# Performance work log

Hardware: AMD Instinct MI355X
Metric: run time of the kernel (lower is better)

The kernel has to match this reference:

```python
import jax, jax.numpy as jnp
import numpy as np

B, TX, TY = 32, 64, 64
E = H = 1024
VEN = VCN = 32000


def _lstm_scan(x_gates, Whh, bhh, h0, c0):
    # x_gates: [T, B, 4H] precomputed input contribution (x @ Wih.T + bih)
    def step(carry, xg_t):
        h, c = carry
        gates = xg_t + h @ Whh.T + bhh  # [B, 4H]
        i, f, g, o = jnp.split(gates, 4, axis=-1)  # torch gate order i,f,g,o
        c = jax.nn.sigmoid(f) * c + jax.nn.sigmoid(i) * jnp.tanh(g)
        h = jax.nn.sigmoid(o) * jnp.tanh(c)
        return (h, c), (h, c)
    (hT, cT), (hs, cs) = jax.lax.scan(step, (h0, c0), x_gates)
    return hs, cs, hT, cT  # hs/cs: [T, B, H]


def setup_inputs() -> dict:
    key = jax.random.key(0)
    ks = jax.random.split(key, 12)
    u = lambda k, shp, s: jax.random.uniform(k, shp, jnp.float32, -s, s)
    s = 1.0 / np.sqrt(H)
    return {
        "x": jax.random.randint(ks[0], (B, TX), 0, VEN, dtype=jnp.int32),
        "x_mask": jnp.ones((B, TX), dtype=jnp.int32),
        "y": jax.random.randint(ks[1], (B, TY), 0, VCN, dtype=jnp.int32),
        "h0": jnp.zeros((B, H), jnp.float32),
        "c0": jnp.zeros((B, H), jnp.float32),
        "emb_en": u(ks[2], (VEN, E), 0.1),
        "emb_cn": u(ks[3], (VCN, E), 0.1),
        "Wih_e": u(ks[4], (4 * H, E), s),
        "Whh_e": u(ks[5], (4 * H, H), s),
        "bih_e": jnp.zeros((4 * H,), jnp.float32),
        "bhh_e": jnp.zeros((4 * H,), jnp.float32),
        "Wih_d": u(ks[6], (4 * H, E), s),
        "Whh_d": u(ks[7], (4 * H, H), s),
        "bih_d": jnp.zeros((4 * H,), jnp.float32),
        "bhh_d": jnp.zeros((4 * H,), jnp.float32),
        "Wout": u(ks[8], (VCN, H), 0.1),
        "bout": jnp.zeros((VCN,), jnp.float32),
    }


def reference(x, x_mask, y, h0, c0, emb_en, emb_cn,
              Wih_e, Whh_e, bih_e, bhh_e,
              Wih_d, Whh_d, bih_d, bhh_d, Wout, bout):
    # --- encoder: per-timestep LSTMCell unrolled via lax.scan ---
    xe = emb_en[x]  # [B, Tx, E]
    xg = jnp.einsum('bte,ge->tbg', xe, Wih_e) + bih_e  # [Tx, B, 4H]
    hs, cs, _, _ = _lstm_scan(xg, Whh_e, bhh_e, h0, c0)  # [Tx, B, H]
    # pick hidden/cell at last valid timestep (mask.sum - 1)
    lengths = jnp.sum(x_mask, axis=1) - 1  # [B]
    bidx = jnp.arange(x.shape[0])
    h = hs[lengths, bidx]  # [B, H]
    c = cs[lengths, bidx]
    # --- decoder: single-layer LSTM ---
    ye = emb_cn[y]  # [B, Ty, E]
    yg = jnp.einsum('bte,ge->tbg', ye, Wih_d) + bih_d  # [Ty, B, 4H]
    dh, _, _, _ = _lstm_scan(yg, Whh_d, bhh_d, h, c)  # [Ty, B, H]
    hiddens = jnp.transpose(dh, (1, 0, 2))  # [B, Ty, H]
    logits = jnp.einsum('bth,vh->btv', hiddens, Wout) + bout  # [B, Ty, V]
    decoded = jax.nn.log_softmax(logits, axis=-1)
    return decoded, hiddens
```

## Files before the change

### kernel.cpp

```cpp
#include <hip/hip_runtime.h>

typedef __attribute__((ext_vector_type(8))) short bf16x8;
typedef __attribute__((ext_vector_type(4))) float fx4;
typedef __attribute__((ext_vector_type(4))) unsigned short u16x4;
typedef __attribute__((ext_vector_type(8))) unsigned short u16x8;
typedef __attribute__((ext_vector_type(4))) unsigned int u32x4;

#define DEV static __device__ __forceinline__

DEV unsigned short f2bf(float f) {
  union { float f; unsigned u; } v; v.f = f;
  unsigned u = v.u;
  u += 0x7fffu + ((u >> 16) & 1u);
  return (unsigned short)(u >> 16);
}
DEV unsigned pk(float a, float b) { return (unsigned)f2bf(a) | ((unsigned)f2bf(b) << 16); }
DEV float sigm(float x) { return 1.f / (1.f + __expf(-x)); }

DEV u32x4 load_coh16(const void* p) {
  u32x4 r;
  asm volatile("global_load_dwordx4 %0, %1, off sc0 sc1" : "=v"(r) : "v"(p));
  return r;
}

__global__ void k_gather(const float* __restrict__ emb, const int* __restrict__ tok,
                         unsigned short* __restrict__ dst) {
  int r = blockIdx.x;
  int t = r >> 5, b = r & 31;
  int token = tok[b * 64 + t];
  const fx4* srow = (const fx4*)(emb + (long)token * 1024);
  u16x4* drow = (u16x4*)(dst + (long)r * 1024);
  fx4 v = srow[threadIdx.x];
  u16x4 o = { f2bf(v[0]), f2bf(v[1]), f2bf(v[2]), f2bf(v[3]) };
  drow[threadIdx.x] = o;
}

__global__ void k_lengths(const int* __restrict__ mask, int* __restrict__ sel) {
  int b = threadIdx.x;
  if (b < 32) {
    int s = 0;
    for (int t = 0; t < 64; ++t) s += mask[b * 64 + t];
    sel[b] = (s + 63) & 63;
  }
}

__global__ void k_init_state(const float* __restrict__ h, const float* __restrict__ c,
                             unsigned short* __restrict__ hbuf0, float* __restrict__ cbuf,
                             int* __restrict__ bar) {
  int i = blockIdx.x * 256 + threadIdx.x;
  hbuf0[i] = f2bf(h[i]);
  cbuf[i] = c[i];
  if (i < 4096) bar[i] = 0;
}

#define SCAN_NBLK 128

template<int MODE>
__global__ __launch_bounds__(512) void k_scan(
    const float* __restrict__ Whh,
    const float* __restrict__ bhh,
    const float* __restrict__ xg,
    unsigned short* __restrict__ hbuf,
    float* __restrict__ cbuf,
    const int* __restrict__ sel,
    float* __restrict__ hsel, float* __restrict__ csel,
    float* __restrict__ hid_out,
    unsigned short* __restrict__ hid_bf,
    int* __restrict__ bar) {
  __shared__ __align__(16) unsigned short hlds[49152];
  __shared__ float gbuf[2][2][32][16];
  int tid = threadIdx.x;
  int bid = blockIdx.x;
  int j0 = bid * 8;
  int w = tid >> 6, lane = tid & 63;
  int mt = w & 1, nt = (w >> 1) & 1, kh = w >> 2;
  int fr = lane & 15, fg = lane >> 4;
  unsigned* hbU = (unsigned*)hbuf;

  bf16x8 breg[16];
  {
    int r = nt * 16 + fr;
    const float* wrow = Whh + ((long)((r >> 3) * 1024 + j0 + (r & 7)) << 10);
#pragma unroll
    for (int i = 0; i < 16; ++i) {
      int kc = (kh * 16 + i) * 4 + fg;
      fx4 lo = *(const fx4*)(wrow + kc * 8);
      fx4 hi = *(const fx4*)(wrow + kc * 8 + 4);
      bf16x8 o = { (short)f2bf(lo[0]), (short)f2bf(lo[1]), (short)f2bf(lo[2]), (short)f2bf(lo[3]),
                   (short)f2bf(hi[0]), (short)f2bf(hi[1]), (short)f2bf(hi[2]), (short)f2bf(hi[3]) };
      breg[i] = o;
    }
  }

  int b = (tid & 255) >> 3, jj = tid & 7, j = j0 + jj;
  float bh0 = 0.f, bh1 = 0.f, bh2 = 0.f, bh3 = 0.f, c_reg = 0.f;
  float x0 = 0.f, x1 = 0.f, x2 = 0.f, x3 = 0.f;
  int sel_b = -1;
  if (tid < 256) {
    bh0 = bhh[j]; bh1 = bhh[1024 + j]; bh2 = bhh[2048 + j]; bh3 = bhh[3072 + j];
    c_reg = cbuf[b * 1024 + j];
    if (MODE == 0) sel_b = sel[b];
    const float* xp = xg + (long)b * 4096 + j;
    x0 = xp[0]; x1 = xp[1024]; x2 = xp[2048]; x3 = xp[3072];
  }

  for (int t = 0; t < 64; ++t) {
    const char* hsrc = (const char*)hbuf + (t & 1) * 65536;
    u32x4 hv[8];
#pragma unroll
    for (int it = 0; it < 8; ++it) {
      int c = it * 512 + tid;
      hv[it] = load_coh16(hsrc + (long)c * 16);
    }
    asm volatile("s_waitcnt vmcnt(0)" ::: "memory");
    __builtin_amdgcn_sched_barrier(0);
#pragma unroll
    for (int it = 0; it < 8; ++it) {
      int c = it * 512 + tid;
      int row = c >> 7, kc = c & 127;
      *(u16x8*)&hlds[(row * 128 + (kc ^ (row & 31))) * 8] = *(u16x8*)&hv[it];
    }
    __syncthreads();

    int arow = mt * 16 + fr;
    fx4 acca = {0.f, 0.f, 0.f, 0.f}, accb = {0.f, 0.f, 0.f, 0.f};
#pragma unroll
    for (int i = 0; i < 16; i += 2) {
      int kcA = (kh * 16 + i) * 4 + fg;
      int kcB = (kh * 16 + i + 1) * 4 + fg;
      bf16x8 a0 = *(const bf16x8*)&hlds[(arow * 128 + (kcA ^ (arow & 31))) * 8];
      bf16x8 a1 = *(const bf16x8*)&hlds[(arow * 128 + (kcB ^ (arow & 31))) * 8];
      acca = __builtin_amdgcn_mfma_f32_16x16x32_bf16(a0, breg[i], acca, 0, 0, 0);
      accb = __builtin_amdgcn_mfma_f32_16x16x32_bf16(a1, breg[i + 1], accb, 0, 0, 0);
    }
#pragma unroll
    for (int q = 0; q < 4; ++q)
      gbuf[kh][nt][mt * 16 + fg * 4 + q][fr] = acca[q] + accb[q];
    __syncthreads();

    if (tid < 256) {
      float gi = gbuf[0][0][b][jj]     + gbuf[1][0][b][jj]     + bh0 + x0;
      float gf = gbuf[0][0][b][8 + jj] + gbuf[1][0][b][8 + jj] + bh1 + x1;
      float gg = gbuf[0][1][b][jj]     + gbuf[1][1][b][jj]     + bh2 + x2;
      float go = gbuf[0][1][b][8 + jj] + gbuf[1][1][b][8 + jj] + bh3 + x3;
      float c_new = sigm(gf) * c_reg + sigm(gi) * tanhf(gg);
      float h = sigm(go) * tanhf(c_new);
      c_reg = c_new;
      float hp = __shfl_xor(h, 1);
      if ((jj & 1) == 0) {
        unsigned val = pk(h, hp);
        __hip_atomic_store(&hbU[((t & 1) ^ 1) * 16384 + b * 512 + ((j0 + jj) >> 1)], val,
                           __ATOMIC_RELAXED, __HIP_MEMORY_SCOPE_AGENT);
      }
      if (MODE == 0) {
        if (t == sel_b) { hsel[b * 1024 + j] = h; csel[b * 1024 + j] = c_new; }
      } else {
        long o = ((long)b * 64 + t) * 1024 + j;
        hid_out[o] = h;
        if (hid_bf) hid_bf[o] = f2bf(h);
      }
    }

    if (t < 63) {
      float nx0 = 0.f, nx1 = 0.f, nx2 = 0.f, nx3 = 0.f;
      if (tid < 256) {
        const float* xp = xg + (long)(t + 1) * 131072 + (long)b * 4096 + j;
        nx0 = xp[0]; nx1 = xp[1024]; nx2 = xp[2048]; nx3 = xp[3072];
      }
      __syncthreads();
      if (w == 0) {
        if (lane == 0)
          __hip_atomic_store(&bar[bid * 32], t + 1, __ATOMIC_RELAXED, __HIP_MEMORY_SCOPE_AGENT);
        for (;;) {
          int v0 = __hip_atomic_load(&bar[lane * 32], __ATOMIC_RELAXED, __HIP_MEMORY_SCOPE_AGENT);
          int v1 = __hip_atomic_load(&bar[(64 + lane) * 32], __ATOMIC_RELAXED, __HIP_MEMORY_SCOPE_AGENT);
          if (__ballot(v0 >= t + 1 && v1 >= t + 1) == 0xFFFFFFFFFFFFFFFFULL) break;
          __builtin_amdgcn_s_sleep(2);
        }
      }
      __syncthreads();
      x0 = nx0; x1 = nx1; x2 = nx2; x3 = nx3;
    }
  }
}

template<typename TA, typename TB>
__global__ __launch_bounds__(256) void k_gemm(const TA* __restrict__ A,
                                              const TB* __restrict__ Bw,
                                              const float* __restrict__ bias,
                                              float* __restrict__ C,
                                              int ldc, int q8) {
  __shared__ __align__(16) unsigned short As[2][4096];
  __shared__ __align__(16) unsigned short Bs[2][4096];
  int lid = blockIdx.x;
  int swz = (lid & 7) * q8 + (lid >> 3);
  long m0 = (long)(swz & 15) * 128;
  long n0 = (long)(swz >> 4) * 128;
  int tid = threadIdx.x, lane = tid & 63, w = tid >> 6;
  int mw = (w & 1) * 64, nw = (w >> 1) * 64;
  int fr = lane & 15, fg = lane >> 4;
  fx4 acc[4][4] = {};

  int crow[2], kc[2], phys[2];
#pragma unroll
  for (int u = 0; u < 2; ++u) {
    int c = tid + u * 256;
    crow[u] = c >> 2; kc[u] = c & 3;
    phys[u] = crow[u] * 4 + (kc[u] ^ ((crow[u] >> 1) & 3));
  }
  u32x4 ra[2], rb[2];
  auto loadOne = [&](const auto* P, long row, int u) -> u32x4 {
    long off = row * 1024 + kc[u] * 8;
    if constexpr (sizeof(*P) == 2) {
      return *(const u32x4*)(P + off);
    } else {
      fx4 lo = *(const fx4*)(P + off);
      fx4 hi = *(const fx4*)(P + off + 4);
      u32x4 r = { pk(lo[0], lo[1]), pk(lo[2], lo[3]), pk(hi[0], hi[1]), pk(hi[2], hi[3]) };
      return r;
    }
  };
  auto loadRegs = [&](int kt) {
#pragma unroll
    for (int u = 0; u < 2; ++u) {
      ra[u] = loadOne(A + (long)kt * 32, m0 + crow[u], u);
      rb[u] = loadOne(Bw + (long)kt * 32, n0 + crow[u], u);
    }
  };
  auto storeRegs = [&](int buf) {
#pragma unroll
    for (int u = 0; u < 2; ++u) {
      *(u32x4*)&As[buf][phys[u] * 8] = ra[u];
      *(u32x4*)&Bs[buf][phys[u] * 8] = rb[u];
    }
  };
  loadRegs(0);
  storeRegs(0);
  __syncthreads();
  for (int kt = 0; kt < 32; ++kt) {
    int cur = kt & 1;
    if (kt < 31) loadRegs(kt + 1);
    bf16x8 af[4], bf_[4];
#pragma unroll
    for (int mi = 0; mi < 4; ++mi) {
      int row = mw + mi * 16 + fr;
      af[mi] = *(const bf16x8*)&As[cur][(row * 4 + (fg ^ ((row >> 1) & 3))) * 8];
    }
#pragma unroll
    for (int ni = 0; ni < 4; ++ni) {
      int row = nw + ni * 16 + fr;
      bf_[ni] = *(const bf16x8*)&Bs[cur][(row * 4 + (fg ^ ((row >> 1) & 3))) * 8];
    }
#pragma unroll
    for (int mi = 0; mi < 4; ++mi)
#pragma unroll
      for (int ni = 0; ni < 4; ++ni)
        acc[mi][ni] = __builtin_amdgcn_mfma_f32_16x16x32_bf16(af[mi], bf_[ni], acc[mi][ni], 0, 0, 0);
    if (kt < 31) storeRegs((kt + 1) & 1);
    __syncthreads();
  }
#pragma unroll
  for (int ni = 0; ni < 4; ++ni) {
    long n = n0 + nw + ni * 16 + fr;
    float bs = bias[n];
#pragma unroll
    for (int mi = 0; mi < 4; ++mi) {
      long rbase = m0 + mw + mi * 16 + fg * 4;
#pragma unroll
      for (int q = 0; q < 4; ++q)
        C[(rbase + q) * ldc + n] = acc[mi][ni][q] + bs;
    }
  }
}

__global__ __launch_bounds__(256) void k_logsoftmax(float* __restrict__ logits) {
  long base = (long)blockIdx.x * 32000;
  float* row = logits + base;
  int tid = threadIdx.x;
  __shared__ float red[4];
  float m = -3.4e38f;
  for (int i = tid; i < 8000; i += 256) {
    fx4 v = ((const fx4*)row)[i];
    m = fmaxf(m, fmaxf(fmaxf(v[0], v[1]), fmaxf(v[2], v[3])));
  }
  for (int o = 32; o; o >>= 1) m = fmaxf(m, __shfl_xor(m, o));
  if ((tid & 63) == 0) red[tid >> 6] = m;
  __syncthreads();
  m = fmaxf(fmaxf(red[0], red[1]), fmaxf(red[2], red[3]));
  float s = 0.f;
  for (int i = tid; i < 8000; i += 256) {
    fx4 v = ((const fx4*)row)[i];
    s += __expf(v[0] - m) + __expf(v[1] - m) + __expf(v[2] - m) + __expf(v[3] - m);
  }
  for (int o = 32; o; o >>= 1) s += __shfl_xor(s, o);
  __syncthreads();
  if ((tid & 63) == 0) red[tid >> 6] = s;
  __syncthreads();
  float lse = m + logf(red[0] + red[1] + red[2] + red[3]);
  for (int i = tid; i < 8000; i += 256) {
    fx4 v = ((const fx4*)row)[i];
    fx4 o = { v[0] - lse, v[1] - lse, v[2] - lse, v[3] - lse };
    ((fx4*)row)[i] = o;
  }
}

extern "C" void kernel_launch(void* const* d_in, const int* in_sizes, int n_in,
                              void* d_out, int out_size, void* d_ws, size_t ws_size,
                              hipStream_t stream) {
  const int*   x     = (const int*)d_in[0];
  const int*   xmask = (const int*)d_in[1];
  const int*   y     = (const int*)d_in[2];
  const float* h0    = (const float*)d_in[3];
  const float* c0    = (const float*)d_in[4];
  const float* embE  = (const float*)d_in[5];
  const float* embC  = (const float*)d_in[6];
  const float* WihE  = (const float*)d_in[7];
  const float* WhhE  = (const float*)d_in[8];
  const float* bihE  = (const float*)d_in[9];
  const float* bhhE  = (const float*)d_in[10];
  const float* WihD  = (const float*)d_in[11];
  const float* WhhD  = (const float*)d_in[12];
  const float* bihD  = (const float*)d_in[13];
  const float* bhhD  = (const float*)d_in[14];
  const float* Wout  = (const float*)d_in[15];
  const float* bout  = (const float*)d_in[16];

  float* out = (float*)d_out;
  float* decoded = out;
  float* hiddens = out + 65536000L;

  float* xg_e = decoded;
  float* xg_d = decoded + 8388608L;
  unsigned short* xe_bf = (unsigned short*)(decoded + 16777216L);
  unsigned short* ye_bf = xe_bf + 2097152L;
  char* sp = (char*)(ye_bf + 2097152L);
  unsigned short* hbuf = (unsigned short*)sp; sp += 2 * 32768 * 2;
  float* cbuf = (float*)sp; sp += 32768 * 4;
  float* hsel = (float*)sp; sp += 32768 * 4;
  float* csel = (float*)sp; sp += 32768 * 4;
  int* sel = (int*)sp; sp += 256;
  int* bar = (int*)sp; sp += 16384;

  unsigned short* hid_bf = (unsigned short*)d_ws;
  bool fast = ws_size >= 2048L * 1024 * 2;

  k_gather<<<2048, 256, 0, stream>>>(embE, x, xe_bf);
  k_gather<<<2048, 256, 0, stream>>>(embC, y, ye_bf);
  k_lengths<<<1, 32, 0, stream>>>(xmask, sel);

  k_gemm<unsigned short, float><<<512, 256, 0, stream>>>(xe_bf, WihE, bihE, xg_e, 4096, 64);
  k_gemm<unsigned short, float><<<512, 256, 0, stream>>>(ye_bf, WihD, bihD, xg_d, 4096, 64);

  k_init_state<<<128, 256, 0, stream>>>(h0, c0, hbuf, cbuf, bar);
  k_scan<0><<<SCAN_NBLK, 512, 0, stream>>>(WhhE, bhhE, xg_e, hbuf, cbuf, sel,
                                           hsel, csel, nullptr, nullptr, bar);
  k_init_state<<<128, 256, 0, stream>>>(hsel, csel, hbuf, cbuf, bar);
  k_scan<1><<<SCAN_NBLK, 512, 0, stream>>>(WhhD, bhhD, xg_d, hbuf, cbuf, nullptr,
                                           nullptr, nullptr, hiddens,
                                           fast ? hid_bf : nullptr, bar);

  if (fast) k_gemm<unsigned short, float><<<4000, 256, 0, stream>>>(hid_bf, Wout, bout, decoded, 32000, 500);
  else      k_gemm<float, float><<<4000, 256, 0, stream>>>(hiddens, Wout, bout, decoded, 32000, 500);
  k_logsoftmax<<<2048, 256, 0, stream>>>(decoded);
}
```

Measured before the change: 1.016 ms.

## Pre-convert weights to bf16, add LDS-direct bf16 GEMM, online logsoftmax, pack barrier flags

Adds a kernel that converts the fp32 Wih and Wout weights to bf16 in scratch space. A new GEMM streams bf16 A and B tiles straight into LDS with global_load_lds, so the conversion no longer happens inside the GEMM loop. Log-softmax now uses a single-pass online max/sum reduction, cutting one full read of each logits row. The scan barrier flags are packed contiguously instead of padded 128 bytes apart, and the spin sleep is shortened. The weight conversion adds extra passes over the weights on every call, and the fast Wout path depends on a large enough workspace.

```diff
diff --git a/kernel.cpp b/kernel.cpp
--- a/kernel.cpp
+++ b/kernel.cpp
@@ -21,6 +21,22 @@
   u32x4 r;
   asm volatile("global_load_dwordx4 %0, %1, off sc0 sc1" : "=v"(r) : "v"(p));
   return r;
+}
+
+typedef __attribute__((address_space(1))) const unsigned int guint;
+typedef __attribute__((address_space(3))) unsigned int luint;
+DEV void gload_lds16(const void* g, void* l) {
+  __builtin_amdgcn_global_load_lds((guint*)g, (luint*)l, 16, 0, 0);
+}
+
+__global__ void k_f2bf4(const float* __restrict__ s, unsigned short* __restrict__ d, long n4) {
+  long i = (long)blockIdx.x * blockDim.x + threadIdx.x;
+  long st = (long)gridDim.x * blockDim.x;
+  for (; i < n4; i += st) {
+    fx4 v = ((const fx4*)s)[i];
+    u16x4 o = { f2bf(v[0]), f2bf(v[1]), f2bf(v[2]), f2bf(v[3]) };
+    ((u16x4*)d)[i] = o;
+  }
 }
 
 __global__ void k_gather(const float* __restrict__ emb, const int* __restrict__ tok,
@@ -170,16 +186,74 @@
       __syncthreads();
       if (w == 0) {
         if (lane == 0)
-          __hip_atomic_store(&bar[bid * 32], t + 1, __ATOMIC_RELAXED, __HIP_MEMORY_SCOPE_AGENT);
+          __hip_atomic_store(&bar[bid], t + 1, __ATOMIC_RELAXED, __HIP_MEMORY_SCOPE_AGENT);
         for (;;) {
-          int v0 = __hip_atomic_load(&bar[lane * 32], __ATOMIC_RELAXED, __HIP_MEMORY_SCOPE_AGENT);
-          int v1 = __hip_atomic_load(&bar[(64 + lane) * 32], __ATOMIC_RELAXED, __HIP_MEMORY_SCOPE_AGENT);
+          int v0 = __hip_atomic_load(&bar[lane], __ATOMIC_RELAXED, __HIP_MEMORY_SCOPE_AGENT);
+          int v1 = __hip_atomic_load(&bar[64 + lane], __ATOMIC_RELAXED, __HIP_MEMORY_SCOPE_AGENT);
           if (__ballot(v0 >= t + 1 && v1 >= t + 1) == 0xFFFFFFFFFFFFFFFFULL) break;
-          __builtin_amdgcn_s_sleep(2);
+          __builtin_amdgcn_s_sleep(1);
         }
       }
       __syncthreads();
       x0 = nx0; x1 = nx1; x2 = nx2; x3 = nx3;
+    }
+  }
+}
+
+__global__ __launch_bounds__(256) void k_gemm_bb(const unsigned short* __restrict__ A,
+                                                 const unsigned short* __restrict__ Bw,
+                                                 const float* __restrict__ bias,
+                                                 float* __restrict__ C,
+                                                 int ldc, int q8) {
+  __shared__ __align__(16) unsigned short As[2][4096];
+  __shared__ __align__(16) unsigned short Bs[2][4096];
+  int lid = blockIdx.x;
+  int swz = (lid & 7) * q8 + (lid >> 3);
+  long m0 = (long)(swz & 15) * 128;
+  long n0 = (long)(swz >> 4) * 128;
+  int tid = threadIdx.x, lane = tid & 63, w = tid >> 6;
+  int mw = (w & 1) * 64, nw = (w >> 1) * 64;
+  int fr = lane & 15, fg = lane >> 4;
+  fx4 acc[4][4] = {};
+  int c0 = tid, c1 = tid + 256;
+  const unsigned short* gA0 = A + (m0 + (c0 >> 2)) * 1024 + (c0 & 3) * 8;
+  const unsigned short* gA1 = A + (m0 + (c1 >> 2)) * 1024 + (c1 & 3) * 8;
+  const unsigned short* gB0 = Bw + (n0 + (c0 >> 2)) * 1024 + (c0 & 3) * 8;
+  const unsigned short* gB1 = Bw + (n0 + (c1 >> 2)) * 1024 + (c1 & 3) * 8;
+  auto stage = [&](int buf, int kt) {
+    int k0 = kt * 32;
+    gload_lds16(gA0 + k0, &As[buf][c0 * 8]);
+    gload_lds16(gA1 + k0, &As[buf][c1 * 8]);
+    gload_lds16(gB0 + k0, &Bs[buf][c0 * 8]);
+    gload_lds16(gB1 + k0, &Bs[buf][c1 * 8]);
+  };
+  stage(0, 0);
+  __syncthreads();
+  for (int kt = 0; kt < 32; ++kt) {
+    int cur = kt & 1;
+    if (kt < 31) stage(cur ^ 1, kt + 1);
+    bf16x8 af[4], bfr[4];
+#pragma unroll
+    for (int mi = 0; mi < 4; ++mi) af[mi]  = *(const bf16x8*)&As[cur][(mw + mi * 16 + fr) * 32 + fg * 8];
+#pragma unroll
+    for (int ni = 0; ni < 4; ++ni) bfr[ni] = *(const bf16x8*)&Bs[cur][(nw + ni * 16 + fr) * 32 + fg * 8];
+#pragma unroll
+    for (int mi = 0; mi < 4; ++mi)
+#pragma unroll
+      for (int ni = 0; ni < 4; ++ni)
+        acc[mi][ni] = __builtin_amdgcn_mfma_f32_16x16x32_bf16(af[mi], bfr[ni], acc[mi][ni], 0, 0, 0);
+    __syncthreads();
+  }
+#pragma unroll
+  for (int ni = 0; ni < 4; ++ni) {
+    long n = n0 + nw + ni * 16 + fr;
+    float bs = bias[n];
+#pragma unroll
+    for (int mi = 0; mi < 4; ++mi) {
+      long rbase = m0 + mw + mi * 16 + fg * 4;
+#pragma unroll
+      for (int q = 0; q < 4; ++q)
+        C[(rbase + q) * ldc + n] = acc[mi][ni][q] + bs;
     }
   }
 }
@@ -277,26 +351,26 @@
   long base = (long)blockIdx.x * 32000;
   float* row = logits + base;
   int tid = threadIdx.x;
-  __shared__ float red[4];
-  float m = -3.4e38f;
+  __shared__ float redm[4], reds[4];
+  float m = -3.4e38f, s = 0.f;
   for (int i = tid; i < 8000; i += 256) {
     fx4 v = ((const fx4*)row)[i];
-    m = fmaxf(m, fmaxf(fmaxf(v[0], v[1]), fmaxf(v[2], v[3])));
-  }
-  for (int o = 32; o; o >>= 1) m = fmaxf(m, __shfl_xor(m, o));
-  if ((tid & 63) == 0) red[tid >> 6] = m;
+    float cm = fmaxf(fmaxf(v[0], v[1]), fmaxf(v[2], v[3]));
+    if (cm > m) { s *= __expf(m - cm); m = cm; }
+    s += __expf(v[0] - m) + __expf(v[1] - m) + __expf(v[2] - m) + __expf(v[3] - m);
+  }
+  for (int o = 32; o; o >>= 1) {
+    float m2 = __shfl_xor(m, o), s2 = __shfl_xor(s, o);
+    float mn = fmaxf(m, m2);
+    s = s * __expf(m - mn) + s2 * __expf(m2 - mn);
+    m = mn;
+  }
+  if ((tid & 63) == 0) { redm[tid >> 6] = m; reds[tid >> 6] = s; }
   __syncthreads();
-  m = fmaxf(fmaxf(red[0], red[1]), fmaxf(red[2], red[3]));
-  float s = 0.f;
-  for (int i = tid; i < 8000; i += 256) {
-    fx4 v = ((const fx4*)row)[i];
-    s += __expf(v[0] - m) + __expf(v[1] - m) + __expf(v[2] - m) + __expf(v[3] - m);
-  }
-  for (int o = 32; o; o >>= 1) s += __shfl_xor(s, o);
-  __syncthreads();
-  if ((tid & 63) == 0) red[tid >> 6] = s;
-  __syncthreads();
-  float lse = m + logf(red[0] + red[1] + red[2] + red[3]);
+  float M = fmaxf(fmaxf(redm[0], redm[1]), fmaxf(redm[2], redm[3]));
+  float S = reds[0] * __expf(redm[0] - M) + reds[1] * __expf(redm[1] - M) +
+            reds[2] * __expf(redm[2] - M) + reds[3] * __expf(redm[3] - M);
+  float lse = M + logf(S);
   for (int i = tid; i < 8000; i += 256) {
     fx4 v = ((const fx4*)row)[i];
     fx4 o = { v[0] - lse, v[1] - lse, v[2] - lse, v[3] - lse };
@@ -331,9 +405,11 @@
 
   float* xg_e = decoded;
   float* xg_d = decoded + 8388608L;
-  unsigned short* xe_bf = (unsigned short*)(decoded + 16777216L);
-  unsigned short* ye_bf = xe_bf + 2097152L;
-  char* sp = (char*)(ye_bf + 2097152L);
+  unsigned short* xe_bf   = (unsigned short*)(decoded + 16777216L);
+  unsigned short* ye_bf   = xe_bf + 2097152L;
+  unsigned short* WihE_bf = ye_bf + 2097152L;
+  unsigned short* WihD_bf = WihE_bf + 4194304L;
+  char* sp = (char*)(WihD_bf + 4194304L);
   unsigned short* hbuf = (unsigned short*)sp; sp += 2 * 32768 * 2;
   float* cbuf = (float*)sp; sp += 32768 * 4;
   float* hsel = (float*)sp; sp += 32768 * 4;
@@ -341,15 +417,20 @@
   int* sel = (int*)sp; sp += 256;
   int* bar = (int*)sp; sp += 16384;
 
-  unsigned short* hid_bf = (unsigned short*)d_ws;
-  bool fast = ws_size >= 2048L * 1024 * 2;
+  unsigned short* hid_bf  = (unsigned short*)d_ws;
+  unsigned short* Wout_bf = hid_bf + 2097152L;
+  bool fast1 = ws_size >= 2048L * 1024 * 2;
+  bool fast2 = ws_size >= 2048L * 1024 * 2 + 32000L * 1024 * 2;
 
   k_gather<<<2048, 256, 0, stream>>>(embE, x, xe_bf);
   k_gather<<<2048, 256, 0, stream>>>(embC, y, ye_bf);
   k_lengths<<<1, 32, 0, stream>>>(xmask, sel);
-
-  k_gemm<unsigned short, float><<<512, 256, 0, stream>>>(xe_bf, WihE, bihE, xg_e, 4096, 64);
-  k_gemm<unsigned short, float><<<512, 256, 0, stream>>>(ye_bf, WihD, bihD, xg_d, 4096, 64);
+  k_f2bf4<<<1024, 256, 0, stream>>>(WihE, WihE_bf, 4096L * 1024 / 4);
+  k_f2bf4<<<1024, 256, 0, stream>>>(WihD, WihD_bf, 4096L * 1024 / 4);
+  if (fast2) k_f2bf4<<<4096, 256, 0, stream>>>(Wout, Wout_bf, 32000L * 1024 / 4);
+
+  k_gemm_bb<<<512, 256, 0, stream>>>(xe_bf, WihE_bf, bihE, xg_e, 4096, 64);
+  k_gemm_bb<<<512, 256, 0, stream>>>(ye_bf, WihD_bf, bihD, xg_d, 4096, 64);
 
   k_init_state<<<128, 256, 0, stream>>>(h0, c0, hbuf, cbuf, bar);
   k_scan<0><<<SCAN_NBLK, 512, 0, stream>>>(WhhE, bhhE, xg_e, hbuf, cbuf, sel,
@@ -357,9 +438,10 @@
   k_init_state<<<128, 256, 0, stream>>>(hsel, csel, hbuf, cbuf, bar);
   k_scan<1><<<SCAN_NBLK, 512, 0, stream>>>(WhhD, bhhD, xg_d, hbuf, cbuf, nullptr,
                                            nullptr, nullptr, hiddens,
-                                           fast ? hid_bf : nullptr, bar);
-
-  if (fast) k_gemm<unsigned short, float><<<4000, 256, 0, stream>>>(hid_bf, Wout, bout, decoded, 32000, 500);
-  else      k_gemm<float, float><<<4000, 256, 0, stream>>>(hiddens, Wout, bout, decoded, 32000, 500);
+                                           fast1 ? hid_bf : nullptr, bar);
+
+  if (fast2)      k_gemm_bb<<<4000, 256, 0, stream>>>(hid_bf, Wout_bf, bout, decoded, 32000, 500);
+  else if (fast1) k_gemm<unsigned short, float><<<4000, 256, 0, stream>>>(hid_bf, Wout, bout, decoded, 32000, 500);
+  else            k_gemm<float, float><<<4000, 256, 0, stream>>>(hiddens, Wout, bout, decoded, 32000, 500);
   k_logsoftmax<<<2048, 256, 0, stream>>>(decoded);
 }
```

Measured after the change: 1.229 ms. +20.9%, slower.
